# Kernel optimization log

Hardware: AMD Instinct MI355X
Metric: run time of the kernel (lower is better)

The kernel has to match this reference:

```python
import jax, jax.numpy as jnp
import numpy as np

def setup_inputs() -> dict:
    key = jax.random.key(0)
    k1, k2 = jax.random.split(key)
    pcs1 = jax.random.normal(k1, (8, 4096, 3), dtype=jnp.float32)
    pcs2 = jax.random.normal(k2, (8, 4096, 3), dtype=jnp.float32)
    return {"pcs1": pcs1, "pcs2": pcs2}

def reference(pcs1, pcs2):
    # Pairwise squared L2 distances: [B, N, M]
    # ||a-b||^2 = ||a||^2 + ||b||^2 - 2 a.b
    sq1 = jnp.sum(pcs1 * pcs1, axis=-1)                # [B, N]
    sq2 = jnp.sum(pcs2 * pcs2, axis=-1)                # [B, M]
    inner = jnp.einsum('bnd,bmd->bnm', pcs1, pcs2)     # [B, N, M]
    d = sq1[:, :, None] + sq2[:, None, :] - 2.0 * inner
    d = jnp.maximum(d, 0.0)  # guard tiny negatives from cancellation
    dist1 = jnp.min(d, axis=2)   # [B, N] nearest in pcs2 for each point of pcs1
    dist2 = jnp.min(d, axis=1)   # [B, M] nearest in pcs1 for each point of pcs2
    loss1 = jnp.mean(jnp.sqrt(dist1))
    loss2 = jnp.mean(jnp.sqrt(dist2))
    return (loss1 + loss2) * 0.5
```

## Files before the change

### kernel.cpp

```cpp
#include <hip/hip_runtime.h>
#include <math.h>


typedef __attribute__((ext_vector_type(8)))  short bf16x8;
typedef __attribute__((ext_vector_type(16))) float f32x16;
typedef float f32x2 __attribute__((ext_vector_type(2)));

#define NPTS 4096
#define BATCH 8
#define FRAG_PER_B 8192u

union FragCast { uint4 u; bf16x8 v; };

__device__ __forceinline__ unsigned short f2bf(float f) {
    unsigned u = __float_as_uint(f);
    return (unsigned short)((u + 0x7FFFu + ((u >> 16) & 1u)) >> 16);
}
__device__ __forceinline__ float bf2f(unsigned short h) {
    return __uint_as_float(((unsigned)h) << 16);
}
__device__ __forceinline__ unsigned pk(unsigned short a, unsigned short b) {
    return (unsigned)a | ((unsigned)b << 16);
}

__global__ __launch_bounds__(256) void chamfer_prep(
    const float* __restrict__ pcs1, const float* __restrict__ pcs2,
    uint4* __restrict__ fa1, uint4* __restrict__ fb2,
    unsigned* __restrict__ dist1u)
{
    const int gid = blockIdx.x * 256 + threadIdx.x;
    const int b   = gid >> 12;
    const int pt  = gid & 4095;

    dist1u[gid] = 0x7F800000u;

    const int tile = pt >> 5, row = pt & 31;
    const size_t i0 = (size_t)b * FRAG_PER_B + ((size_t)tile * 2 + 0) * 32 + row;
    const size_t i1 = (size_t)b * FRAG_PER_B + ((size_t)tile * 2 + 1) * 32 + row;
    const unsigned short ONE = 0x3F80;

    {
        const float* s = pcs1 + ((size_t)b * NPTS + pt) * 3;
        float x = s[0], y = s[1], z = s[2];
        float sq = fmaf(x, x, fmaf(y, y, z * z));
        float m2x = -2.0f * x, m2y = -2.0f * y, m2z = -2.0f * z;
        unsigned short hx = f2bf(m2x), hy = f2bf(m2y), hz = f2bf(m2z);
        unsigned short lx = f2bf(m2x - bf2f(hx));
        unsigned short ly = f2bf(m2y - bf2f(hy));
        unsigned short lz = f2bf(m2z - bf2f(hz));
        unsigned short sh = f2bf(sq);
        unsigned short sl = f2bf(sq - bf2f(sh));
        fa1[i0] = make_uint4(pk(hx, hy), pk(hz, hx), pk(hy, hz), pk(lx, ly));
        fa1[i1] = make_uint4(pk(lz, lx), pk(ly, lz), pk(sh, sl), pk(ONE, ONE));
    }
    {
        const float* s = pcs2 + ((size_t)b * NPTS + pt) * 3;
        float x = s[0], y = s[1], z = s[2];
        float sq = fmaf(x, x, fmaf(y, y, z * z));
        unsigned short px = f2bf(x), py = f2bf(y), pz = f2bf(z);
        unsigned short qx = f2bf(x - bf2f(px));
        unsigned short qy = f2bf(y - bf2f(py));
        unsigned short qz = f2bf(z - bf2f(pz));
        unsigned short sh = f2bf(sq);
        unsigned short sl = f2bf(sq - bf2f(sh));
        fb2[i0] = make_uint4(pk(px, py), pk(pz, qx), pk(qy, qz), pk(px, py));
        fb2[i1] = make_uint4(pk(pz, qx), pk(qy, qz), pk(ONE, ONE), pk(sh, sl));
    }
}

__global__ __launch_bounds__(512, 2) void chamfer_mfma(
    const uint4* __restrict__ fa1, const uint4* __restrict__ fb2,
    unsigned* __restrict__ dist1u, unsigned* __restrict__ cpart)
{
    __shared__ unsigned ldscol[2048];

    const int bid    = blockIdx.x;
    const int b      = bid >> 5;
    const int rgroup = (bid >> 1) & 15;
    const int chalf  = bid & 1;

    const int tid = threadIdx.x;
    const int w   = tid >> 6;
    const int l   = tid & 63;
    const int hf  = l >> 5;
    const int ln  = l & 31;
    const int rt  = rgroup * 8 + w;

    {
        uint4* lc4 = (uint4*)ldscol;
        lc4[tid] = make_uint4(0x7F800000u, 0x7F800000u, 0x7F800000u, 0x7F800000u);
    }

    FragCast aq;
    aq.u = fa1[(size_t)b * FRAG_PER_B + ((size_t)rt * 2 + hf) * 32 + ln];

    const uint4* bptr = fb2 + (size_t)b * FRAG_PER_B
                        + (size_t)chalf * 64 * 64 + hf * 32 + ln;

    const f32x16 cz = {0.f,0.f,0.f,0.f,0.f,0.f,0.f,0.f,
                       0.f,0.f,0.f,0.f,0.f,0.f,0.f,0.f};
    float rmin[16];
#pragma unroll
    for (int i = 0; i < 16; ++i) rmin[i] = 3.4e38f;

    __syncthreads();

    uint4 p0 = bptr[0];
    uint4 p1 = bptr[64];
#pragma unroll 2
    for (int ct = 0; ct < 64; ++ct) {
        FragCast bq; bq.u = p0;
        p0 = p1;
        p1 = bptr[(size_t)(ct + 2) * 64];
        f32x16 D = __builtin_amdgcn_mfma_f32_32x32x16_bf16(aq.v, bq.v, cz, 0, 0, 0);

#pragma unroll
        for (int i = 0; i < 16; ++i) rmin[i] = fminf(rmin[i], D[i]);

        float cm = fminf(D[0], D[1]);
#pragma unroll
        for (int i = 1; i < 8; ++i)
            cm = fminf(fminf(cm, D[2 * i]), D[2 * i + 1]);
        cm = fmaxf(cm, 0.0f);
        atomicMin(&ldscol[ct * 32 + ln], __float_as_uint(cm));
    }

#pragma unroll
    for (int off = 1; off < 32; off <<= 1) {
#pragma unroll
        for (int i = 0; i < 16; ++i)
            rmin[i] = fminf(rmin[i], __shfl_xor(rmin[i], off, 64));
    }
    float v = 3.4e38f;
#pragma unroll
    for (int reg = 0; reg < 16; ++reg)
        if (ln == reg) v = rmin[reg];
    if (ln < 16) {
        const int row = (ln & 3) + 8 * (ln >> 2) + 4 * hf;
        atomicMin(&dist1u[(size_t)b * NPTS + rt * 32 + row],
                  __float_as_uint(fmaxf(v, 0.0f)));
    }

    __syncthreads();
    {
        const uint4* lc4 = (const uint4*)ldscol;
        uint4* dst = (uint4*)&cpart[(((size_t)(b * 2 + chalf) * 16 + rgroup) * 2048)];
        dst[tid] = lc4[tid];
    }
}

__global__ __launch_bounds__(256) void chamfer_red1(
    const unsigned* __restrict__ dist1u, const unsigned* __restrict__ cpart,
    float* __restrict__ bpart)
{
    __shared__ float ws[4];
    const int t  = threadIdx.x;
    const int tg = blockIdx.x * 256 + t;
    const int b  = tg >> 12;
    const int c  = tg & 4095;
    const int chalf = c >> 11, cl = c & 2047;

    unsigned m = 0xFFFFFFFFu;
    const unsigned* base = &cpart[(size_t)(b * 2 + chalf) * 16 * 2048 + cl];
#pragma unroll
    for (int rg = 0; rg < 16; ++rg)
        m = min(m, base[(size_t)rg * 2048]);

    float s = sqrtf(__uint_as_float(m)) + sqrtf(__uint_as_float(dist1u[tg]));
#pragma unroll
    for (int off = 1; off < 64; off <<= 1) s += __shfl_xor(s, off, 64);
    if ((t & 63) == 0) ws[t >> 6] = s;
    __syncthreads();
    if (t == 0)
        bpart[blockIdx.x] = ws[0] + ws[1] + ws[2] + ws[3];
}

__global__ __launch_bounds__(64) void chamfer_red2(
    const float* __restrict__ bpart, float* __restrict__ out)
{
    float v = bpart[threadIdx.x] + bpart[threadIdx.x + 64];
#pragma unroll
    for (int off = 1; off < 64; off <<= 1) v += __shfl_xor(v, off, 64);
    if (threadIdx.x == 0) out[0] = v * (1.0f / 65536.0f);
}

#define CPAIRS 1024
#define PA 16
#define RSTRIDE 68

__device__ __forceinline__ f32x2 pk_fma_lo(f32x2 c, f32x2 q, f32x2 acc) {
    f32x2 d;
    asm("v_pk_fma_f32 %0, %1, %2, %3 op_sel:[0,0,0] op_sel_hi:[0,1,1]"
        : "=v"(d) : "v"(c), "v"(q), "v"(acc));
    return d;
}
__device__ __forceinline__ f32x2 pk_fma_hi(f32x2 c, f32x2 q, f32x2 acc) {
    f32x2 d;
    asm("v_pk_fma_f32 %0, %1, %2, %3 op_sel:[1,0,0] op_sel_hi:[1,1,1]"
        : "=v"(d) : "v"(c), "v"(q), "v"(acc));
    return d;
}
__device__ __forceinline__ void vmin3(float& acc, float a, float b) {
    asm("v_min3_f32 %0, %1, %2, %3" : "=v"(acc) : "v"(acc), "v"(a), "v"(b));
}

__global__ __launch_bounds__(256, 4) void chamfer_vec(
    const float* __restrict__ pcs1, const float* __restrict__ pcs2,
    float* __restrict__ partials)
{
    __shared__ float4 lds[2 * CPAIRS];
    float4* bx = lds;
    float4* bz = lds + CPAIRS;

    const int bid = blockIdx.x;
    const int dir = bid >> 9;
    const int b   = (bid >> 6) & 7;
    const int ach = bid & 63;

    const float* A  = dir ? pcs2 : pcs1;
    const float* Bp = dir ? pcs1 : pcs2;
    const float* abase = A  + (size_t)b * NPTS * 3;
    const float* bbase = Bp + (size_t)b * NPTS * 3;

    const int tid = threadIdx.x;
    const int w   = tid >> 6;
    const int l   = tid & 63;

    const int apt = ach * 64 + w * PA;
    f32x2 cx[PA / 2], cy[PA / 2], cz2[PA / 2];
    float tmin[PA];
#pragma unroll
    for (int p2 = 0; p2 < PA / 2; ++p2) {
        const float* s = abase + (size_t)(apt + 2 * p2) * 3;
        cx[p2]  = (f32x2){-2.0f * s[0], -2.0f * s[3]};
        cy[p2]  = (f32x2){-2.0f * s[1], -2.0f * s[4]};
        cz2[p2] = (f32x2){-2.0f * s[2], -2.0f * s[5]};
        tmin[2 * p2] = 3.4e38f; tmin[2 * p2 + 1] = 3.4e38f;
    }

    for (int c = 0; c < 2; ++c) {
        if (c) __syncthreads();
#pragma unroll
        for (int i = 0; i < CPAIRS / 256; ++i) {
            int j  = i * 256 + tid;
            const float* s = bbase + (size_t)(c * CPAIRS + j) * 6;
            float x0 = s[0], y0 = s[1], z0 = s[2];
            float x1 = s[3], y1 = s[4], z1 = s[5];
            bx[j] = make_float4(x0, x1, y0, y1);
            bz[j] = make_float4(z0, z1,
                                fmaf(x0, x0, fmaf(y0, y0, z0 * z0)),
                                fmaf(x1, x1, fmaf(y1, y1, z1 * z1)));
        }
        __syncthreads();
#pragma unroll 4
        for (int t = 0; t < CPAIRS / 64; ++t) {
            float4 X = bx[t * 64 + l];
            float4 Z = bz[t * 64 + l];
            f32x2 qx = (f32x2){X.x, X.y};
            f32x2 qy = (f32x2){X.z, X.w};
            f32x2 qz = (f32x2){Z.x, Z.y};
            f32x2 qw = (f32x2){Z.z, Z.w};
#pragma unroll
            for (int p2 = 0; p2 < PA / 2; ++p2) {
                f32x2 d0 = pk_fma_lo(cz2[p2], qz, qw);
                d0 = pk_fma_lo(cy[p2], qy, d0);
                d0 = pk_fma_lo(cx[p2], qx, d0);
                vmin3(tmin[2 * p2], d0.x, d0.y);
                f32x2 d1 = pk_fma_hi(cz2[p2], qz, qw);
                d1 = pk_fma_hi(cy[p2], qy, d1);
                d1 = pk_fma_hi(cx[p2], qx, d1);
                vmin3(tmin[2 * p2 + 1], d1.x, d1.y);
            }
        }
    }

    __syncthreads();
    float* lds2 = (float*)lds;
#pragma unroll
    for (int p = 0; p < PA; ++p)
        lds2[(w * PA + p) * RSTRIDE + l] = tmin[p];
    __syncthreads();

    if (tid < 64) {
        const int g = tid;
        float m = 3.4e38f;
        const float4* row = (const float4*)&lds2[g * RSTRIDE];
#pragma unroll
        for (int i = 0; i < 16; ++i) {
            float4 v = row[i];
            m = fminf(fminf(m, fminf(v.x, v.y)), fminf(v.z, v.w));
        }
        const int ap = ach * 64 + g;
        float x = abase[ap * 3 + 0], y = abase[ap * 3 + 1], z = abase[ap * 3 + 2];
        float s = sqrtf(fmaxf(fmaf(x, x, fmaf(y, y, z * z)) + m, 0.0f));
#pragma unroll
        for (int off = 1; off < 64; off <<= 1) s += __shfl_xor(s, off, 64);
        if (g == 0) partials[bid] = s;
    }
}

__global__ __launch_bounds__(256) void chamfer_final(
    const float* __restrict__ partials, int n, float scale,
    float* __restrict__ out)
{
    __shared__ float ws[4];
    const int t = threadIdx.x;
    float v = 0.0f;
    for (int i = t; i < n; i += 256) v += partials[i];
#pragma unroll
    for (int off = 1; off < 64; off <<= 1) v += __shfl_xor(v, off, 64);
    if ((t & 63) == 0) ws[t >> 6] = v;
    __syncthreads();
    if (t == 0)
        out[0] = (ws[0] + ws[1] + ws[2] + ws[3]) * scale;
}

extern "C" void kernel_launch(void* const* d_in, const int* in_sizes, int n_in,
                              void* d_out, int out_size, void* d_ws, size_t ws_size,
                              hipStream_t stream) {
    const float* pcs1 = (const float*)d_in[0];
    const float* pcs2 = (const float*)d_in[1];
    float* out = (float*)d_out;

    const size_t MB = 1048576;
    const size_t need = 2 * MB + 128 * 1024 + 2 * MB + 4096;

    if (ws_size >= need) {
        char* w = (char*)d_ws;
        uint4*    fa1    = (uint4*)(w);
        uint4*    fb2    = (uint4*)(w + 1 * MB);
        unsigned* dist1u = (unsigned*)(w + 2 * MB);
        unsigned* cpart  = (unsigned*)(w + 2 * MB + 128 * 1024);
        float*    bpart  = (float*)(w + 4 * MB + 128 * 1024);

        chamfer_prep<<<dim3(128), dim3(256), 0, stream>>>(
            pcs1, pcs2, fa1, fb2, dist1u);
        chamfer_mfma<<<dim3(256), dim3(512), 0, stream>>>(
            fa1, fb2, dist1u, cpart);
        chamfer_red1<<<dim3(128), dim3(256), 0, stream>>>(dist1u, cpart, bpart);
        chamfer_red2<<<dim3(1),   dim3(64),  0, stream>>>(bpart, out);
    } else {
        float* partials = (float*)d_ws;
        chamfer_vec  <<<dim3(1024), dim3(256), 0, stream>>>(pcs1, pcs2, partials);
        chamfer_final<<<dim3(1),    dim3(256), 0, stream>>>(
            partials, 1024, 1.0f / 65536.0f, out);
    }
}
```

Before: 28.05 us.

## Split MFMA columns into quarters and fuse final reduction via atomic counter

The MFMA distance kernel now splits each batch's columns into four quarters instead of two. That doubles the grid to 512 blocks and halves the per-block loop and LDS column buffer, with launch bounds raised to allow more resident blocks. The separate final reduction kernel is removed: the first reduction kernel uses a last-block-done atomic counter, reset in the prep kernel, to sum the partials and write the output. This trades one kernel launch and better CU occupancy for more atomicMin traffic on dist1u and a serial 128-element sum in one thread.

```diff
diff --git a/kernel.cpp b/kernel.cpp
--- a/kernel.cpp
+++ b/kernel.cpp
@@ -26,9 +26,10 @@
 __global__ __launch_bounds__(256) void chamfer_prep(
     const float* __restrict__ pcs1, const float* __restrict__ pcs2,
     uint4* __restrict__ fa1, uint4* __restrict__ fb2,
-    unsigned* __restrict__ dist1u)
+    unsigned* __restrict__ dist1u, unsigned* __restrict__ counter)
 {
     const int gid = blockIdx.x * 256 + threadIdx.x;
+    if (gid == 0) *counter = 0u;
     const int b   = gid >> 12;
     const int pt  = gid & 4095;
 
@@ -68,16 +69,16 @@
     }
 }
 
-__global__ __launch_bounds__(512, 2) void chamfer_mfma(
+__global__ __launch_bounds__(512, 4) void chamfer_mfma(
     const uint4* __restrict__ fa1, const uint4* __restrict__ fb2,
     unsigned* __restrict__ dist1u, unsigned* __restrict__ cpart)
 {
-    __shared__ unsigned ldscol[2048];
+    __shared__ unsigned ldscol[1024];
 
     const int bid    = blockIdx.x;
-    const int b      = bid >> 5;
-    const int rgroup = (bid >> 1) & 15;
-    const int chalf  = bid & 1;
+    const int b      = bid >> 6;
+    const int rgroup = (bid >> 2) & 15;
+    const int cq     = bid & 3;
 
     const int tid = threadIdx.x;
     const int w   = tid >> 6;
@@ -86,16 +87,13 @@
     const int ln  = l & 31;
     const int rt  = rgroup * 8 + w;
 
-    {
-        uint4* lc4 = (uint4*)ldscol;
-        lc4[tid] = make_uint4(0x7F800000u, 0x7F800000u, 0x7F800000u, 0x7F800000u);
-    }
+    ((uint2*)ldscol)[tid] = make_uint2(0x7F800000u, 0x7F800000u);
 
     FragCast aq;
     aq.u = fa1[(size_t)b * FRAG_PER_B + ((size_t)rt * 2 + hf) * 32 + ln];
 
     const uint4* bptr = fb2 + (size_t)b * FRAG_PER_B
-                        + (size_t)chalf * 64 * 64 + hf * 32 + ln;
+                        + (size_t)cq * 2048 + hf * 32 + ln;
 
     const f32x16 cz = {0.f,0.f,0.f,0.f,0.f,0.f,0.f,0.f,
                        0.f,0.f,0.f,0.f,0.f,0.f,0.f,0.f};
@@ -108,7 +106,7 @@
     uint4 p0 = bptr[0];
     uint4 p1 = bptr[64];
 #pragma unroll 2
-    for (int ct = 0; ct < 64; ++ct) {
+    for (int ct = 0; ct < 32; ++ct) {
         FragCast bq; bq.u = p0;
         p0 = p1;
         p1 = bptr[(size_t)(ct + 2) * 64];
@@ -117,10 +115,17 @@
 #pragma unroll
         for (int i = 0; i < 16; ++i) rmin[i] = fminf(rmin[i], D[i]);
 
-        float cm = fminf(D[0], D[1]);
-#pragma unroll
-        for (int i = 1; i < 8; ++i)
-            cm = fminf(fminf(cm, D[2 * i]), D[2 * i + 1]);
+        float a0 = fminf(D[0],  D[1]);
+        float a1 = fminf(D[2],  D[3]);
+        float a2 = fminf(D[4],  D[5]);
+        float a3 = fminf(D[6],  D[7]);
+        float a4 = fminf(D[8],  D[9]);
+        float a5 = fminf(D[10], D[11]);
+        float a6 = fminf(D[12], D[13]);
+        float a7 = fminf(D[14], D[15]);
+        float b0 = fminf(a0, a1), b1 = fminf(a2, a3);
+        float b2 = fminf(a4, a5), b3 = fminf(a6, a7);
+        float cm = fminf(fminf(b0, b1), fminf(b2, b3));
         cm = fmaxf(cm, 0.0f);
         atomicMin(&ldscol[ct * 32 + ln], __float_as_uint(cm));
     }
@@ -142,46 +147,48 @@
     }
 
     __syncthreads();
-    {
-        const uint4* lc4 = (const uint4*)ldscol;
-        uint4* dst = (uint4*)&cpart[(((size_t)(b * 2 + chalf) * 16 + rgroup) * 2048)];
-        dst[tid] = lc4[tid];
+    if (tid < 256) {
+        uint4 vv = ((const uint4*)ldscol)[tid];
+        ((uint4*)&cpart[((size_t)(b * 4 + cq) * 16 + rgroup) * 1024])[tid] = vv;
     }
 }
 
 __global__ __launch_bounds__(256) void chamfer_red1(
     const unsigned* __restrict__ dist1u, const unsigned* __restrict__ cpart,
-    float* __restrict__ bpart)
-{
-    __shared__ float ws[4];
+    float* __restrict__ bpart, unsigned* __restrict__ counter,
+    float* __restrict__ out)
+{
+    __shared__ float ws4[4];
     const int t  = threadIdx.x;
     const int tg = blockIdx.x * 256 + t;
     const int b  = tg >> 12;
     const int c  = tg & 4095;
-    const int chalf = c >> 11, cl = c & 2047;
+    const int cq = c >> 10, cl = c & 1023;
 
     unsigned m = 0xFFFFFFFFu;
-    const unsigned* base = &cpart[(size_t)(b * 2 + chalf) * 16 * 2048 + cl];
-#pragma unroll
-    for (int rg = 0; rg < 16; ++rg)
-        m = min(m, base[(size_t)rg * 2048]);
+    const unsigned* base = &cpart[((size_t)(b * 4 + cq) * 16) * 1024 + cl];
+#pragma unroll
+    for (int rg = 0; rg < 16; ++rg) {
+        unsigned u = base[(size_t)rg * 1024];
+        m = (u < m) ? u : m;
+    }
 
     float s = sqrtf(__uint_as_float(m)) + sqrtf(__uint_as_float(dist1u[tg]));
 #pragma unroll
     for (int off = 1; off < 64; off <<= 1) s += __shfl_xor(s, off, 64);
-    if ((t & 63) == 0) ws[t >> 6] = s;
-    __syncthreads();
-    if (t == 0)
-        bpart[blockIdx.x] = ws[0] + ws[1] + ws[2] + ws[3];
-}
-
-__global__ __launch_bounds__(64) void chamfer_red2(
-    const float* __restrict__ bpart, float* __restrict__ out)
-{
-    float v = bpart[threadIdx.x] + bpart[threadIdx.x + 64];
-#pragma unroll
-    for (int off = 1; off < 64; off <<= 1) v += __shfl_xor(v, off, 64);
-    if (threadIdx.x == 0) out[0] = v * (1.0f / 65536.0f);
+    if ((t & 63) == 0) ws4[t >> 6] = s;
+    __syncthreads();
+    if (t == 0) {
+        bpart[blockIdx.x] = ws4[0] + ws4[1] + ws4[2] + ws4[3];
+        __threadfence();
+        unsigned old = atomicAdd(counter, 1u);
+        if (old == 127u) {
+            __threadfence();
+            float tot = 0.0f;
+            for (int i = 0; i < 128; ++i) tot += bpart[i];
+            out[0] = tot * (1.0f / 65536.0f);
+        }
+    }
 }
 
 #define CPAIRS 1024
@@ -303,16 +310,16 @@
     const float* __restrict__ partials, int n, float scale,
     float* __restrict__ out)
 {
-    __shared__ float ws[4];
+    __shared__ float ws4[4];
     const int t = threadIdx.x;
     float v = 0.0f;
     for (int i = t; i < n; i += 256) v += partials[i];
 #pragma unroll
     for (int off = 1; off < 64; off <<= 1) v += __shfl_xor(v, off, 64);
-    if ((t & 63) == 0) ws[t >> 6] = v;
+    if ((t & 63) == 0) ws4[t >> 6] = v;
     __syncthreads();
     if (t == 0)
-        out[0] = (ws[0] + ws[1] + ws[2] + ws[3]) * scale;
+        out[0] = (ws4[0] + ws4[1] + ws4[2] + ws4[3]) * scale;
 }
 
 extern "C" void kernel_launch(void* const* d_in, const int* in_sizes, int n_in,
@@ -323,22 +330,23 @@
     float* out = (float*)d_out;
 
     const size_t MB = 1048576;
-    const size_t need = 2 * MB + 128 * 1024 + 2 * MB + 4096;
+    const size_t need = 4 * MB + 128 * 1024 + 4096;
 
     if (ws_size >= need) {
         char* w = (char*)d_ws;
-        uint4*    fa1    = (uint4*)(w);
-        uint4*    fb2    = (uint4*)(w + 1 * MB);
-        unsigned* dist1u = (unsigned*)(w + 2 * MB);
-        unsigned* cpart  = (unsigned*)(w + 2 * MB + 128 * 1024);
-        float*    bpart  = (float*)(w + 4 * MB + 128 * 1024);
+        uint4*    fa1     = (uint4*)(w);
+        uint4*    fb2     = (uint4*)(w + 1 * MB);
+        unsigned* dist1u  = (unsigned*)(w + 2 * MB);
+        unsigned* cpart   = (unsigned*)(w + 2 * MB + 128 * 1024);
+        float*    bpart   = (float*)(w + 4 * MB + 128 * 1024);
+        unsigned* counter = (unsigned*)(w + 4 * MB + 128 * 1024 + 512);
 
         chamfer_prep<<<dim3(128), dim3(256), 0, stream>>>(
-            pcs1, pcs2, fa1, fb2, dist1u);
-        chamfer_mfma<<<dim3(256), dim3(512), 0, stream>>>(
+            pcs1, pcs2, fa1, fb2, dist1u, counter);
+        chamfer_mfma<<<dim3(512), dim3(512), 0, stream>>>(
             fa1, fb2, dist1u, cpart);
-        chamfer_red1<<<dim3(128), dim3(256), 0, stream>>>(dist1u, cpart, bpart);
-        chamfer_red2<<<dim3(1),   dim3(64),  0, stream>>>(bpart, out);
+        chamfer_red1<<<dim3(128), dim3(256), 0, stream>>>(
+            dist1u, cpart, bpart, counter, out);
     } else {
         float* partials = (float*)d_ws;
         chamfer_vec  <<<dim3(1024), dim3(256), 0, stream>>>(pcs1, pcs2, partials);
```

Result: slower. 32.17 us (+14.7%).
